# Kernel tuning notes

Measured on AMD Instinct MI355X. Metric: run time of the kernel, lower is better.

Reference implementation:

```python
import jax, jax.numpy as jnp
import numpy as np

B, N, M = 8, 8192, 2048
C1, C2 = 128, 256
MLP = [256, 128]
EPS_W = 1e-8   # inverse-distance epsilon
EPS_BN = 1e-5  # batchnorm epsilon


def setup_inputs() -> dict:
    key = jax.random.key(0)
    ks = jax.random.split(key, 12)
    inp = {
        "xyz1": jax.random.normal(ks[0], (B, N, 3), jnp.float32),
        "xyz2": jax.random.normal(ks[1], (B, M, 3), jnp.float32),
        "points1": jax.random.normal(ks[2], (B, N, C1), jnp.float32),
        "points2": jax.random.normal(ks[3], (B, M, C2), jnp.float32),
    }
    last = C1 + C2
    for i, out_c in enumerate(MLP):
        inp[f"W{i}"] = jax.random.normal(ks[4 + 2 * i], (out_c, last), jnp.float32) * (1.0 / np.sqrt(last))
        inp[f"b{i}"] = jnp.zeros((out_c,), jnp.float32)
        inp[f"gamma{i}"] = jnp.ones((out_c,), jnp.float32)
        inp[f"beta{i}"] = jnp.zeros((out_c,), jnp.float32)
        last = out_c
    return inp


def _square_distance(src, dst):
    # [B,N,M] squared euclidean distances
    d = -2.0 * jnp.einsum("bnc,bmc->bnm", src, dst)
    d = d + jnp.sum(src * src, -1)[:, :, None]
    d = d + jnp.sum(dst * dst, -1)[:, None, :]
    return d


def _fp_forward(xyz1, xyz2, points1, points2, params):
    dists = _square_distance(xyz1, xyz2)              # [B,N,M]
    neg_top, idx = jax.lax.top_k(-dists, 3)            # 3 smallest distances
    d3 = -neg_top                                      # [B,N,3]
    recip = 1.0 / (d3 + EPS_W)
    weight = recip / jnp.sum(recip, axis=2, keepdims=True)  # [B,N,3]
    gathered = jax.vmap(lambda p, i: p[i])(points2, idx)     # [B,N,3,C2]
    interpolated = jnp.sum(gathered * weight[..., None], axis=2)  # [B,N,C2]
    x = jnp.concatenate([points1, interpolated], axis=-1)        # [B,N,C1+C2]
    for (Wi, bi, gi, bti) in params:
        x = jnp.einsum("bnc,oc->bno", x, Wi) + bi
        # BatchNorm1d (training mode): stats over batch and point dims
        mean = jnp.mean(x, axis=(0, 1))
        var = jnp.var(x, axis=(0, 1))
        x = (x - mean) * jax.lax.rsqrt(var + EPS_BN) * gi + bti
        x = jax.nn.relu(x)
    return x  # [B,N,MLP[-1]]


def reference(xyz1, xyz2, points1, points2, W0, b0, gamma0, beta0, W1, b1, gamma1, beta1):
    params = [(W0, b0, gamma0, beta0), (W1, b1, gamma1, beta1)]
    return _fp_forward(xyz1, xyz2, points1, points2, params)
```

## Files before the change

kernel.cpp:

```cpp
#include <hip/hip_runtime.h>
#include <cstdint>
#include <cstddef>

#define BATCH 8
#define NPTS  8192
#define MPTS  2048
#define C1    128
#define C2    256
#define K0    384
#define O0    256
#define O1    128
#define NROWS (BATCH * NPTS)

typedef __attribute__((ext_vector_type(8))) short bf16x8;
typedef __attribute__((ext_vector_type(4))) float f32x4;

__device__ __forceinline__ unsigned short f2b(float f) {
    union { float f; unsigned int u; } v; v.f = f;
    unsigned int u = v.u + 0x7FFFu + ((v.u >> 16) & 1u);
    return (unsigned short)(u >> 16);
}
__device__ __forceinline__ float b2f(unsigned short h) {
    union { unsigned int u; float f; } v; v.u = ((unsigned int)h) << 16; return v.f;
}
__device__ __forceinline__ unsigned int pack2(float a, float b) {
    return (unsigned int)f2b(a) | ((unsigned int)f2b(b) << 16);
}
__device__ __forceinline__ float med3(float a, float b, float c) {
    return __builtin_amdgcn_fmed3f(a, b, c);
}

__device__ __forceinline__ void merge3(float x0, float x1, float x2,
                                       int ix0, int ix1, int ix2,
                                       float y0, float y1, float y2,
                                       int iy0, int iy1, int iy2,
                                       float& z0, float& z1, float& z2,
                                       int& iz0, int& iz1, int& iz2) {
    const bool c0 = y0 < x0;
    const bool c1a = y1 < x0;
    const bool c1b = y0 < x1;
    z0 = c0 ? y0 : x0;  iz0 = c0 ? iy0 : ix0;
    const float z1A = c1a ? y1 : x0; const int iz1A = c1a ? iy1 : ix0;
    const float z1B = c1b ? y0 : x1; const int iz1B = c1b ? iy0 : ix1;
    z1 = c0 ? z1A : z1B; iz1 = c0 ? iz1A : iz1B;
    const bool mA1c = y2 < x0;
    const bool mA2c = y1 < x1;
    const bool mB2c = y0 < x2;
    const float mA1 = mA1c ? y2 : x0; const int imA1 = mA1c ? iy2 : ix0;
    const float mA2 = mA2c ? y1 : x1; const int imA2 = mA2c ? iy1 : ix1;
    const float mB2 = mB2c ? y0 : x2; const int imB2 = mB2c ? iy0 : ix2;
    const float z2A = c1a ? mA1 : mA2; const int iz2A = c1a ? imA1 : imA2;
    const float z2B = c1b ? mA2 : mB2; const int iz2B = c1b ? imA2 : imB2;
    z2 = c0 ? z2A : z2B; iz2 = c0 ? iz2A : iz2B;
}

__global__ __launch_bounds__(512) void k_knn(const float* __restrict__ xyz1,
                                             const float* __restrict__ xyz2,
                                             int* __restrict__ idxo,
                                             float* __restrict__ wo) {
    __shared__ float4 s2p[16][129];

    const int b = blockIdx.x >> 7;
    const int qbase = (blockIdx.x & 127) * 64;

    for (int p = threadIdx.x; p < MPTS; p += 512) {
        const size_t src = ((size_t)b * MPTS + p) * 3;
        float px = xyz2[src + 0], py = xyz2[src + 1], pz = xyz2[src + 2];
        float sy = __fadd_rn(__fadd_rn(__fmul_rn(px, px), __fmul_rn(py, py)),
                             __fmul_rn(pz, pz));
        s2p[p >> 7][p & 127] = make_float4(-2.0f * px, -2.0f * py, -2.0f * pz, sy);
    }
    __syncthreads();

    const int qp  = threadIdx.x >> 4;
    const int seg = threadIdx.x & 15;
    const int nA = qbase + qp * 2;
    const size_t qoffA = ((size_t)b * NPTS + nA) * 3;
    const float ax = xyz1[qoffA + 0], ay = xyz1[qoffA + 1], az = xyz1[qoffA + 2];
    const float bx = xyz1[qoffA + 3], by = xyz1[qoffA + 4], bz = xyz1[qoffA + 5];
    const float sA = __fadd_rn(__fadd_rn(__fmul_rn(ax, ax), __fmul_rn(ay, ay)),
                               __fmul_rn(az, az));
    const float sB = __fadd_rn(__fadd_rn(__fmul_rn(bx, bx), __fmul_rn(by, by)),
                               __fmul_rn(bz, bz));

    float a0 = 3.0e38f, a1 = 3.0e38f, a2 = 3.0e38f;
    float e0 = 3.0e38f, e1 = 3.0e38f, e2 = 3.0e38f;
    int ai0 = 0, ai1 = 0, ai2 = 0;
    int bi0 = 0, bi1 = 0, bi2 = 0;
    const int m0 = seg * 128;
    const float4* segp = &s2p[seg][0];
#pragma unroll 8
    for (int mm = 0; mm < 128; ++mm) {
        const float4 pp = segp[mm];
        float tA = __fadd_rn(__fadd_rn(__fmul_rn(ax, pp.x), __fmul_rn(ay, pp.y)),
                             __fmul_rn(az, pp.z));
        float dA = __fadd_rn(__fadd_rn(tA, sA), pp.w);
        float tB = __fadd_rn(__fadd_rn(__fmul_rn(bx, pp.x), __fmul_rn(by, pp.y)),
                             __fmul_rn(bz, pp.z));
        float dB = __fadd_rn(__fadd_rn(tB, sB), pp.w);
        {
            const bool c0 = dA < a0, c1 = dA < a1, c2 = dA < a2;
            ai2 = c2 ? (c1 ? ai1 : mm) : ai2;
            ai1 = c1 ? (c0 ? ai0 : mm) : ai1;
            ai0 = c0 ? mm : ai0;
            float n2 = med3(dA, a1, a2), n1 = med3(dA, a0, a1), n0 = fminf(dA, a0);
            a2 = n2; a1 = n1; a0 = n0;
        }
        {
            const bool c0 = dB < e0, c1 = dB < e1, c2 = dB < e2;
            bi2 = c2 ? (c1 ? bi1 : mm) : bi2;
            bi1 = c1 ? (c0 ? bi0 : mm) : bi1;
            bi0 = c0 ? mm : bi0;
            float n2 = med3(dB, e1, e2), n1 = med3(dB, e0, e1), n0 = fminf(dB, e0);
            e2 = n2; e1 = n1; e0 = n0;
        }
    }
    ai0 += m0; ai1 += m0; ai2 += m0;
    bi0 += m0; bi1 += m0; bi2 += m0;

#pragma unroll
    for (int k = 1; k <= 8; k <<= 1) {
        const bool up = (threadIdx.x & k) != 0;
        {
            float p0 = __shfl_xor(a0, k), p1 = __shfl_xor(a1, k), p2 = __shfl_xor(a2, k);
            int   q0 = __shfl_xor(ai0, k), q1 = __shfl_xor(ai1, k), q2 = __shfl_xor(ai2, k);
            float x0 = up ? p0 : a0, x1 = up ? p1 : a1, x2 = up ? p2 : a2;
            int  ix0 = up ? q0 : ai0, ix1 = up ? q1 : ai1, ix2 = up ? q2 : ai2;
            float y0 = up ? a0 : p0, y1 = up ? a1 : p1, y2 = up ? a2 : p2;
            int  iy0 = up ? ai0 : q0, iy1 = up ? ai1 : q1, iy2 = up ? ai2 : q2;
            merge3(x0, x1, x2, ix0, ix1, ix2, y0, y1, y2, iy0, iy1, iy2,
                   a0, a1, a2, ai0, ai1, ai2);
        }
        {
            float p0 = __shfl_xor(e0, k), p1 = __shfl_xor(e1, k), p2 = __shfl_xor(e2, k);
            int   q0 = __shfl_xor(bi0, k), q1 = __shfl_xor(bi1, k), q2 = __shfl_xor(bi2, k);
            float x0 = up ? p0 : e0, x1 = up ? p1 : e1, x2 = up ? p2 : e2;
            int  ix0 = up ? q0 : bi0, ix1 = up ? q1 : bi1, ix2 = up ? q2 : bi2;
            float y0 = up ? e0 : p0, y1 = up ? e1 : p1, y2 = up ? e2 : p2;
            int  iy0 = up ? bi0 : q0, iy1 = up ? bi1 : q1, iy2 = up ? bi2 : q2;
            merge3(x0, x1, x2, ix0, ix1, ix2, y0, y1, y2, iy0, iy1, iy2,
                   e0, e1, e2, bi0, bi1, bi2);
        }
    }

    if (seg == 0) {
        {
            const float r0 = 1.0f / __fadd_rn(a0, 1e-8f);
            const float r1 = 1.0f / __fadd_rn(a1, 1e-8f);
            const float r2 = 1.0f / __fadd_rn(a2, 1e-8f);
            const float norm = __fadd_rn(__fadd_rn(r0, r1), r2);
            const size_t row = (size_t)b * NPTS + nA;
            idxo[row * 3 + 0] = ai0; idxo[row * 3 + 1] = ai1; idxo[row * 3 + 2] = ai2;
            wo[row * 3 + 0] = r0 / norm;
            wo[row * 3 + 1] = r1 / norm;
            wo[row * 3 + 2] = r2 / norm;
        }
        {
            const float r0 = 1.0f / __fadd_rn(e0, 1e-8f);
            const float r1 = 1.0f / __fadd_rn(e1, 1e-8f);
            const float r2 = 1.0f / __fadd_rn(e2, 1e-8f);
            const float norm = __fadd_rn(__fadd_rn(r0, r1), r2);
            const size_t row = (size_t)b * NPTS + nA + 1;
            idxo[row * 3 + 0] = bi0; idxo[row * 3 + 1] = bi1; idxo[row * 3 + 2] = bi2;
            wo[row * 3 + 0] = r0 / norm;
            wo[row * 3 + 1] = r1 / norm;
            wo[row * 3 + 2] = r2 / norm;
        }
    }
}

__global__ __launch_bounds__(256) void k_cvt(const float* __restrict__ W0,
                                             const float* __restrict__ W1,
                                             unsigned short* __restrict__ Wb0,
                                             unsigned short* __restrict__ Wb1) {
    const int e = blockIdx.x * 256 + threadIdx.x;
    if (e < O0 * K0) Wb0[e] = f2b(W0[e]);
    const int e2 = e - O0 * K0;
    if (e2 >= 0 && e2 < O1 * O0) Wb1[e2] = f2b(W1[e2]);
}

__global__ __launch_bounds__(512) void k_gemm0(const float* __restrict__ p1,
                                               const float* __restrict__ p2,
                                               const int* __restrict__ idx,
                                               const float* __restrict__ w,
                                               const unsigned short* __restrict__ Wb,
                                               const float* __restrict__ bias,
                                               unsigned short* __restrict__ y,
                                               float* __restrict__ ps,
                                               float* __restrict__ pq) {
    __shared__ __align__(16) unsigned short As[128 * 64];
    __shared__ __align__(16) unsigned short Bs[256 * 64];
    __shared__ float cps[2][256][2];
    const int t = threadIdx.x;
    const int r0 = blockIdx.x * 128;
    const int lane = t & 63;
    const int wid = t >> 6;
    const int wm = wid & 1;
    const int wn = wid >> 1;

    const int row_a = t >> 2;
    const int sa0 = (t & 3) * 2;
    const int row_b = t >> 1;
    const int sb0 = (t & 1) * 4;

    const int grow = r0 + row_a;
    const int bb = grow >> 13;
    const int i0 = idx[grow * 3 + 0];
    const int i1 = idx[grow * 3 + 1];
    const int i2 = idx[grow * 3 + 2];
    const float w0 = w[grow * 3 + 0];
    const float w1 = w[grow * 3 + 1];
    const float w2 = w[grow * 3 + 2];
    const float* pbase = p2 + (size_t)bb * MPTS * C2;
    const float* g0 = pbase + (size_t)i0 * C2;
    const float* g1 = pbase + (size_t)i1 * C2;
    const float* g2 = pbase + (size_t)i2 * C2;
    const float* p1row = p1 + (size_t)grow * C1;

    const unsigned short* bptr = Wb + (size_t)row_b * K0;
    unsigned short* asw = &As[row_a * 64];
    unsigned short* bsw = &Bs[row_b * 64];
    const int swa = row_a & 7;
    const int swb = row_b & 7;

    f32x4 zero = {0.f, 0.f, 0.f, 0.f};
    f32x4 acc[4][4];
#pragma unroll
    for (int i = 0; i < 4; ++i)
#pragma unroll
        for (int j = 0; j < 4; ++j) acc[i][j] = zero;

    for (int kt = 0; kt < K0; kt += 64) {
#pragma unroll
        for (int i = 0; i < 2; ++i) {
            const int slot = sa0 + i;
            const int gc = kt + slot * 8;
            uint4 ov;
            if (kt < C1) {
                const float4 u = *(const float4*)&p1row[gc];
                const float4 v = *(const float4*)&p1row[gc + 4];
                ov.x = pack2(u.x, u.y); ov.y = pack2(u.z, u.w);
                ov.z = pack2(v.x, v.y); ov.w = pack2(v.z, v.w);
            } else {
                const int cc = gc - C1;
                const float4 u0 = *(const float4*)&g0[cc];
                const float4 u1 = *(const float4*)&g0[cc + 4];
                const float4 v0 = *(const float4*)&g1[cc];
                const float4 v1 = *(const float4*)&g1[cc + 4];
                const float4 t0 = *(const float4*)&g2[cc];
                const float4 t1 = *(const float4*)&g2[cc + 4];
                const float f0 = w0 * u0.x + w1 * v0.x + w2 * t0.x;
                const float f1 = w0 * u0.y + w1 * v0.y + w2 * t0.y;
                const float f2 = w0 * u0.z + w1 * v0.z + w2 * t0.z;
                const float f3 = w0 * u0.w + w1 * v0.w + w2 * t0.w;
                const float f4 = w0 * u1.x + w1 * v1.x + w2 * t1.x;
                const float f5 = w0 * u1.y + w1 * v1.y + w2 * t1.y;
                const float f6 = w0 * u1.z + w1 * v1.z + w2 * t1.z;
                const float f7 = w0 * u1.w + w1 * v1.w + w2 * t1.w;
                ov.x = pack2(f0, f1); ov.y = pack2(f2, f3);
                ov.z = pack2(f4, f5); ov.w = pack2(f6, f7);
            }
            *(uint4*)(asw + ((slot ^ swa) * 8)) = ov;
        }
#pragma unroll
        for (int i = 0; i < 4; ++i) {
            const int slot = sb0 + i;
            *(uint4*)(bsw + (slot ^ swb) * 8) = *(const uint4*)(bptr + kt + slot * 8);
        }
        __syncthreads();
#pragma unroll
        for (int ks = 0; ks < 2; ++ks) {
            bf16x8 af[4], bfr[4];
#pragma unroll
            for (int fr = 0; fr < 4; ++fr) {
                const int row = wm * 64 + fr * 16 + (lane & 15);
                const int slot = (ks * 4 + (lane >> 4)) ^ (row & 7);
                af[fr] = *(const bf16x8*)&As[row * 64 + slot * 8];
            }
#pragma unroll
            for (int fc = 0; fc < 4; ++fc) {
                const int row = wn * 64 + fc * 16 + (lane & 15);
                const int slot = (ks * 4 + (lane >> 4)) ^ (row & 7);
                bfr[fc] = *(const bf16x8*)&Bs[row * 64 + slot * 8];
            }
#pragma unroll
            for (int fr = 0; fr < 4; ++fr)
#pragma unroll
                for (int fc = 0; fc < 4; ++fc)
                    acc[fr][fc] = __builtin_amdgcn_mfma_f32_16x16x32_bf16(
                        af[fr], bfr[fc], acc[fr][fc], 0, 0, 0);
        }
        __syncthreads();
    }

    float bv[4];
#pragma unroll
    for (int fc = 0; fc < 4; ++fc) {
        const int n = wn * 64 + fc * 16 + (lane & 15);
        bv[fc] = bias[n];
        float s = 0.0f, q = 0.0f;
#pragma unroll
        for (int fr = 0; fr < 4; ++fr) {
#pragma unroll
            for (int j = 0; j < 4; ++j) {
                const float v = b2f(f2b(acc[fr][fc][j] + bv[fc]));
                s += v;
                q = fmaf(v, v, q);
            }
        }
        s += __shfl_xor(s, 16); s += __shfl_xor(s, 32);
        q += __shfl_xor(q, 16); q += __shfl_xor(q, 32);
        if ((lane >> 4) == 0) { cps[wm][n][0] = s; cps[wm][n][1] = q; }
    }
    __syncthreads();
    if (t < 256) {
        const float s = cps[0][t][0] + cps[1][t][0];
        const float q = cps[0][t][1] + cps[1][t][1];
        const size_t o = (size_t)blockIdx.x * 256 + t;
        ps[o] = s; pq[o] = q;
    }

#pragma unroll
    for (int p = 0; p < 2; ++p) {
        __syncthreads();
        if (wm == p) {
#pragma unroll
            for (int fc = 0; fc < 4; ++fc) {
                const int n = wn * 64 + fc * 16 + (lane & 15);
#pragma unroll
                for (int fr = 0; fr < 4; ++fr) {
#pragma unroll
                    for (int j = 0; j < 4; ++j) {
                        const int lr = fr * 16 + (lane >> 4) * 4 + j;
                        Bs[lr * 256 + n] = f2b(acc[fr][fc][j] + bv[fc]);
                    }
                }
            }
        }
        __syncthreads();
        const int lr2 = t >> 3;
        const int cb = (t & 7);
#pragma unroll
        for (int i = 0; i < 4; ++i) {
            const int col = (cb + i * 8) * 8;
            *(uint4*)&y[(size_t)(r0 + p * 64 + lr2) * O0 + col] =
                *(const uint4*)&Bs[lr2 * 256 + col];
        }
    }
}

__global__ __launch_bounds__(256) void k_fin0(const float* __restrict__ ps,
                                              const float* __restrict__ pq,
                                              const float* __restrict__ gamma,
                                              const float* __restrict__ beta,
                                              float* __restrict__ sc,
                                              float* __restrict__ sh) {
    __shared__ float red[8][32][2];
    const int tid = threadIdx.x;
    const int cl = tid & 31, qr = tid >> 5;
    const int c = blockIdx.x * 32 + cl;
    float s = 0.0f, q = 0.0f;
    for (int bx = qr * 64; bx < qr * 64 + 64; ++bx) {
        s += ps[(size_t)bx * 256 + c];
        q += pq[(size_t)bx * 256 + c];
    }
    red[qr][cl][0] = s; red[qr][cl][1] = q;
    __syncthreads();
    if (tid < 32) {
        float ss = 0.0f, qq = 0.0f;
#pragma unroll
        for (int k = 0; k < 8; ++k) { ss += red[k][tid][0]; qq += red[k][tid][1]; }
        const int ch = blockIdx.x * 32 + tid;
        const float mean = ss * (1.0f / NROWS);
        const float var = qq * (1.0f / NROWS) - mean * mean;
        const float rs = rsqrtf(var + 1e-5f);
        const float scale = gamma[ch] * rs;
        sc[ch] = scale;
        sh[ch] = beta[ch] - mean * scale;
    }
}

__global__ __launch_bounds__(256) void k_gemm1(const unsigned short* __restrict__ y0,
                                               const unsigned short* __restrict__ Wb,
                                               const float* __restrict__ bias,
                                               const float* __restrict__ sc,
                                               const float* __restrict__ sh,
                                               unsigned short* __restrict__ y1,
                                               float* __restrict__ ps,
                                               float* __restrict__ pq) {
    __shared__ __align__(16) unsigned short As[128 * 64];
    __shared__ __align__(16) unsigned short Bs[128 * 64];
    __shared__ float cps[2][128][2];
    const int t = threadIdx.x;
    const int r0 = blockIdx.x * 128;
    const int lane = t & 63;
    const int wm = (t >> 6) & 1;
    const int wn = (t >> 6) >> 1;
    const int row_s = t >> 1;
    const int slot4 = (t & 1) * 4;
    const int sw = row_s & 7;

    const unsigned short* aptr = y0 + (size_t)(r0 + row_s) * O0;
    const unsigned short* bptr = Wb + (size_t)row_s * O0;
    unsigned short* asw = &As[row_s * 64];
    unsigned short* bsw = &Bs[row_s * 64];

    f32x4 zero = {0.f, 0.f, 0.f, 0.f};
    f32x4 acc[4][4];
#pragma unroll
    for (int i = 0; i < 4; ++i)
#pragma unroll
        for (int j = 0; j < 4; ++j) acc[i][j] = zero;

    for (int kt = 0; kt < O0; kt += 64) {
#pragma unroll
        for (int i = 0; i < 4; ++i) {
            const int slot = slot4 + i;
            const int ssw = slot ^ sw;
            const int c0 = kt + slot * 8;
            uint4 av = *(const uint4*)(aptr + c0);
            const float4 s0 = *(const float4*)&sc[c0];
            const float4 s1 = *(const float4*)&sc[c0 + 4];
            const float4 h0 = *(const float4*)&sh[c0];
            const float4 h1 = *(const float4*)&sh[c0 + 4];
            uint4 ov;
            {
                float v0 = b2f(av.x & 0xffff), v1 = b2f(av.x >> 16);
                ov.x = pack2(fmaxf(fmaf(v0, s0.x, h0.x), 0.f),
                             fmaxf(fmaf(v1, s0.y, h0.y), 0.f));
                float v2 = b2f(av.y & 0xffff), v3 = b2f(av.y >> 16);
                ov.y = pack2(fmaxf(fmaf(v2, s0.z, h0.z), 0.f),
                             fmaxf(fmaf(v3, s0.w, h0.w), 0.f));
                float v4 = b2f(av.z & 0xffff), v5 = b2f(av.z >> 16);
                ov.z = pack2(fmaxf(fmaf(v4, s1.x, h1.x), 0.f),
                             fmaxf(fmaf(v5, s1.y, h1.y), 0.f));
                float v6 = b2f(av.w & 0xffff), v7 = b2f(av.w >> 16);
                ov.w = pack2(fmaxf(fmaf(v6, s1.z, h1.z), 0.f),
                             fmaxf(fmaf(v7, s1.w, h1.w), 0.f));
            }
            *(uint4*)(asw + ssw * 8) = ov;
            uint4 bv = *(const uint4*)(bptr + c0);
            *(uint4*)(bsw + ssw * 8) = bv;
        }
        __syncthreads();
#pragma unroll
        for (int ks = 0; ks < 2; ++ks) {
            bf16x8 af[4], bfr[4];
#pragma unroll
            for (int fr = 0; fr < 4; ++fr) {
                const int row = wm * 64 + fr * 16 + (lane & 15);
                const int slot = (ks * 4 + (lane >> 4)) ^ (row & 7);
                af[fr] = *(const bf16x8*)&As[row * 64 + slot * 8];
            }
#pragma unroll
            for (int fc = 0; fc < 4; ++fc) {
                const int row = wn * 64 + fc * 16 + (lane & 15);
                const int slot = (ks * 4 + (lane >> 4)) ^ (row & 7);
                bfr[fc] = *(const bf16x8*)&Bs[row * 64 + slot * 8];
            }
#pragma unroll
            for (int fr = 0; fr < 4; ++fr)
#pragma unroll
                for (int fc = 0; fc < 4; ++fc)
                    acc[fr][fc] = __builtin_amdgcn_mfma_f32_16x16x32_bf16(
                        af[fr], bfr[fc], acc[fr][fc], 0, 0, 0);
        }
        __syncthreads();
    }

    float bvr[4];
#pragma unroll
    for (int fc = 0; fc < 4; ++fc) {
        const int cl = wn * 64 + fc * 16 + (lane & 15);
        bvr[fc] = bias[cl];
        float s = 0.0f, q = 0.0f;
#pragma unroll
        for (int fr = 0; fr < 4; ++fr) {
#pragma unroll
            for (int j = 0; j < 4; ++j) {
                const float v = b2f(f2b(acc[fr][fc][j] + bvr[fc]));
                s += v;
                q = fmaf(v, v, q);
            }
        }
        s += __shfl_xor(s, 16); s += __shfl_xor(s, 32);
        q += __shfl_xor(q, 16); q += __shfl_xor(q, 32);
        if ((lane >> 4) == 0) { cps[wm][cl][0] = s; cps[wm][cl][1] = q; }
    }
    __syncthreads();
    if (t < 128) {
        ps[(size_t)blockIdx.x * 128 + t] = cps[0][t][0] + cps[1][t][0];
        pq[(size_t)blockIdx.x * 128 + t] = cps[0][t][1] + cps[1][t][1];
    }

#pragma unroll
    for (int p = 0; p < 2; ++p) {
        __syncthreads();
        if (wm == p) {
#pragma unroll
            for (int fc = 0; fc < 4; ++fc) {
                const int cl = wn * 64 + fc * 16 + (lane & 15);
#pragma unroll
                for (int fr = 0; fr < 4; ++fr) {
#pragma unroll
                    for (int j = 0; j < 4; ++j) {
                        const int lr = fr * 16 + (lane >> 4) * 4 + j;
                        Bs[lr * 128 + cl] = f2b(acc[fr][fc][j] + bvr[fc]);
                    }
                }
            }
        }
        __syncthreads();
        const int lr2 = t >> 2;
        const int cb = (t & 3);
#pragma unroll
        for (int i = 0; i < 4; ++i) {
            const int col = (cb + i * 4) * 8;
            *(uint4*)&y1[(size_t)(r0 + p * 64 + lr2) * O1 + col] =
                *(const uint4*)&Bs[lr2 * 128 + col];
        }
    }
}

__global__ __launch_bounds__(128) void k_fin1(const float* __restrict__ ps,
                                              const float* __restrict__ pq,
                                              const float* __restrict__ gamma,
                                              const float* __restrict__ beta,
                                              float* __restrict__ sc,
                                              float* __restrict__ sh) {
    __shared__ float red[8][16][2];
    const int tid = threadIdx.x;
    const int cl = tid & 15, qr = tid >> 4;
    const int c = blockIdx.x * 16 + cl;
    float s = 0.0f, q = 0.0f;
    for (int bx = qr * 64; bx < qr * 64 + 64; ++bx) {
        s += ps[(size_t)bx * 128 + c];
        q += pq[(size_t)bx * 128 + c];
    }
    red[qr][cl][0] = s; red[qr][cl][1] = q;
    __syncthreads();
    if (tid < 16) {
        float ss = 0.0f, qq = 0.0f;
#pragma unroll
        for (int k = 0; k < 8; ++k) { ss += red[k][tid][0]; qq += red[k][tid][1]; }
        const int ch = blockIdx.x * 16 + tid;
        const float mean = ss * (1.0f / NROWS);
        const float var = qq * (1.0f / NROWS) - mean * mean;
        const float rs = rsqrtf(var + 1e-5f);
        const float scale = gamma[ch] * rs;
        sc[ch] = scale;
        sh[ch] = beta[ch] - mean * scale;
    }
}

__global__ __launch_bounds__(256) void k_bnrelu(const unsigned short* __restrict__ y1,
                                                const float* __restrict__ sc,
                                                const float* __restrict__ sh,
                                                float* __restrict__ out) {
    const int e8 = blockIdx.x * 256 + threadIdx.x;
    const int c = (e8 & 15) << 3;
    const uint4 v = ((const uint4*)y1)[e8];
    float4 lo, hi;
    const float4 s0 = *(const float4*)&sc[c];
    const float4 s1 = *(const float4*)&sc[c + 4];
    const float4 h0 = *(const float4*)&sh[c];
    const float4 h1 = *(const float4*)&sh[c + 4];
    lo.x = fmaxf(fmaf(b2f(v.x & 0xffff), s0.x, h0.x), 0.0f);
    lo.y = fmaxf(fmaf(b2f(v.x >> 16),    s0.y, h0.y), 0.0f);
    lo.z = fmaxf(fmaf(b2f(v.y & 0xffff), s0.z, h0.z), 0.0f);
    lo.w = fmaxf(fmaf(b2f(v.y >> 16),    s0.w, h0.w), 0.0f);
    hi.x = fmaxf(fmaf(b2f(v.z & 0xffff), s1.x, h1.x), 0.0f);
    hi.y = fmaxf(fmaf(b2f(v.z >> 16),    s1.y, h1.y), 0.0f);
    hi.z = fmaxf(fmaf(b2f(v.w & 0xffff), s1.z, h1.z), 0.0f);
    hi.w = fmaxf(fmaf(b2f(v.w >> 16),    s1.w, h1.w), 0.0f);
    ((float4*)out)[(size_t)e8 * 2 + 0] = lo;
    ((float4*)out)[(size_t)e8 * 2 + 1] = hi;
}

extern "C" void kernel_launch(void* const* d_in, const int* in_sizes, int n_in,
                              void* d_out, int out_size, void* d_ws, size_t ws_size,
                              hipStream_t stream) {
    const float* xyz1    = (const float*)d_in[0];
    const float* xyz2    = (const float*)d_in[1];
    const float* points1 = (const float*)d_in[2];
    const float* points2 = (const float*)d_in[3];
    const float* W0      = (const float*)d_in[4];
    const float* b0      = (const float*)d_in[5];
    const float* gamma0  = (const float*)d_in[6];
    const float* beta0   = (const float*)d_in[7];
    const float* W1      = (const float*)d_in[8];
    const float* b1      = (const float*)d_in[9];
    const float* gamma1  = (const float*)d_in[10];
    const float* beta1   = (const float*)d_in[11];
    float* out = (float*)d_out;

    char* ws = (char*)d_ws;
    unsigned short* y0  = (unsigned short*)(ws + 0);
    unsigned short* y1b = (unsigned short*)(ws + 33554432ull);
    int*            idxb= (int*)           (ws + 50331648ull);
    float*          wb  = (float*)         (ws + 51118080ull);
    unsigned short* Wb0 = (unsigned short*)(ws + 51904512ull);
    unsigned short* Wb1 = (unsigned short*)(ws + 52101120ull);
    float*          ps0 = (float*)         (ws + 52166656ull);
    float*          pq0 = (float*)         (ws + 52690944ull);
    float*          ps1 = (float*)         (ws + 53215232ull);
    float*          pq1 = (float*)         (ws + 53477376ull);
    float*          sc0 = (float*)         (ws + 53739520ull);
    float*          sh0 = (float*)         (ws + 53740544ull);
    float*          sc1 = (float*)         (ws + 53741568ull);
    float*          sh1 = (float*)         (ws + 53742080ull);

    hipLaunchKernelGGL(k_cvt, dim3(512), dim3(256), 0, stream, W0, W1, Wb0, Wb1);
    hipLaunchKernelGGL(k_knn, dim3(1024), dim3(512), 0, stream, xyz1, xyz2,
                       idxb, wb);
    hipLaunchKernelGGL(k_gemm0, dim3(NROWS / 128), dim3(512), 0, stream,
                       points1, points2, idxb, wb, Wb0, b0, y0, ps0, pq0);
    hipLaunchKernelGGL(k_fin0, dim3(8), dim3(256), 0, stream,
                       ps0, pq0, gamma0, beta0, sc0, sh0);
    hipLaunchKernelGGL(k_gemm1, dim3(NROWS / 128), dim3(256), 0, stream,
                       y0, Wb1, b1, sc0, sh0, y1b, ps1, pq1);
    hipLaunchKernelGGL(k_fin1, dim3(8), dim3(128), 0, stream,
                       ps1, pq1, gamma1, beta1, sc1, sh1);
    hipLaunchKernelGGL(k_bnrelu, dim3(NROWS * O1 / 8 / 256), dim3(256), 0, stream,
                       y1b, sc1, sh1, out);
}
```

Baseline: 161.7 us.

## Fuse KNN search into first GEMM and convert weights to bf16 on the fly

The separate KNN kernel is folded into the prologue of k_gemm0: each 128-row block loads all xyz2 points of its batch into shared memory, computes the 3 nearest neighbours and weights for its rows, and keeps idx/weights in shared memory instead of going through global memory. The k_cvt weight-conversion kernel is removed, and both GEMMs read fp32 weights and pack them to bf16 while staging tiles. This saves two launches and the idx/weight round trip. In exchange, each block now does more KNN work per thread (8 segments of 256 instead of 16 of 128), the GEMM grid of 512 blocks runs the KNN with less parallelism, and weight conversion is repeated in every block.

```diff
diff --git a/kernel.cpp b/kernel.cpp
--- a/kernel.cpp
+++ b/kernel.cpp
@@ -54,145 +54,135 @@
     z2 = c0 ? z2A : z2B; iz2 = c0 ? iz2A : iz2B;
 }
 
-__global__ __launch_bounds__(512) void k_knn(const float* __restrict__ xyz1,
-                                             const float* __restrict__ xyz2,
-                                             int* __restrict__ idxo,
-                                             float* __restrict__ wo) {
-    __shared__ float4 s2p[16][129];
-
-    const int b = blockIdx.x >> 7;
-    const int qbase = (blockIdx.x & 127) * 64;
-
-    for (int p = threadIdx.x; p < MPTS; p += 512) {
-        const size_t src = ((size_t)b * MPTS + p) * 3;
-        float px = xyz2[src + 0], py = xyz2[src + 1], pz = xyz2[src + 2];
-        float sy = __fadd_rn(__fadd_rn(__fmul_rn(px, px), __fmul_rn(py, py)),
-                             __fmul_rn(pz, pz));
-        s2p[p >> 7][p & 127] = make_float4(-2.0f * px, -2.0f * py, -2.0f * pz, sy);
-    }
-    __syncthreads();
-
-    const int qp  = threadIdx.x >> 4;
-    const int seg = threadIdx.x & 15;
-    const int nA = qbase + qp * 2;
-    const size_t qoffA = ((size_t)b * NPTS + nA) * 3;
-    const float ax = xyz1[qoffA + 0], ay = xyz1[qoffA + 1], az = xyz1[qoffA + 2];
-    const float bx = xyz1[qoffA + 3], by = xyz1[qoffA + 4], bz = xyz1[qoffA + 5];
-    const float sA = __fadd_rn(__fadd_rn(__fmul_rn(ax, ax), __fmul_rn(ay, ay)),
-                               __fmul_rn(az, az));
-    const float sB = __fadd_rn(__fadd_rn(__fmul_rn(bx, bx), __fmul_rn(by, by)),
-                               __fmul_rn(bz, bz));
-
-    float a0 = 3.0e38f, a1 = 3.0e38f, a2 = 3.0e38f;
-    float e0 = 3.0e38f, e1 = 3.0e38f, e2 = 3.0e38f;
-    int ai0 = 0, ai1 = 0, ai2 = 0;
-    int bi0 = 0, bi1 = 0, bi2 = 0;
-    const int m0 = seg * 128;
-    const float4* segp = &s2p[seg][0];
-#pragma unroll 8
-    for (int mm = 0; mm < 128; ++mm) {
-        const float4 pp = segp[mm];
-        float tA = __fadd_rn(__fadd_rn(__fmul_rn(ax, pp.x), __fmul_rn(ay, pp.y)),
-                             __fmul_rn(az, pp.z));
-        float dA = __fadd_rn(__fadd_rn(tA, sA), pp.w);
-        float tB = __fadd_rn(__fadd_rn(__fmul_rn(bx, pp.x), __fmul_rn(by, pp.y)),
-                             __fmul_rn(bz, pp.z));
-        float dB = __fadd_rn(__fadd_rn(tB, sB), pp.w);
-        {
-            const bool c0 = dA < a0, c1 = dA < a1, c2 = dA < a2;
-            ai2 = c2 ? (c1 ? ai1 : mm) : ai2;
-            ai1 = c1 ? (c0 ? ai0 : mm) : ai1;
-            ai0 = c0 ? mm : ai0;
-            float n2 = med3(dA, a1, a2), n1 = med3(dA, a0, a1), n0 = fminf(dA, a0);
-            a2 = n2; a1 = n1; a0 = n0;
-        }
-        {
-            const bool c0 = dB < e0, c1 = dB < e1, c2 = dB < e2;
-            bi2 = c2 ? (c1 ? bi1 : mm) : bi2;
-            bi1 = c1 ? (c0 ? bi0 : mm) : bi1;
-            bi0 = c0 ? mm : bi0;
-            float n2 = med3(dB, e1, e2), n1 = med3(dB, e0, e1), n0 = fminf(dB, e0);
-            e2 = n2; e1 = n1; e0 = n0;
-        }
-    }
-    ai0 += m0; ai1 += m0; ai2 += m0;
-    bi0 += m0; bi1 += m0; bi2 += m0;
-
-#pragma unroll
-    for (int k = 1; k <= 8; k <<= 1) {
-        const bool up = (threadIdx.x & k) != 0;
-        {
-            float p0 = __shfl_xor(a0, k), p1 = __shfl_xor(a1, k), p2 = __shfl_xor(a2, k);
-            int   q0 = __shfl_xor(ai0, k), q1 = __shfl_xor(ai1, k), q2 = __shfl_xor(ai2, k);
-            float x0 = up ? p0 : a0, x1 = up ? p1 : a1, x2 = up ? p2 : a2;
-            int  ix0 = up ? q0 : ai0, ix1 = up ? q1 : ai1, ix2 = up ? q2 : ai2;
-            float y0 = up ? a0 : p0, y1 = up ? a1 : p1, y2 = up ? a2 : p2;
-            int  iy0 = up ? ai0 : q0, iy1 = up ? ai1 : q1, iy2 = up ? ai2 : q2;
-            merge3(x0, x1, x2, ix0, ix1, ix2, y0, y1, y2, iy0, iy1, iy2,
-                   a0, a1, a2, ai0, ai1, ai2);
-        }
-        {
-            float p0 = __shfl_xor(e0, k), p1 = __shfl_xor(e1, k), p2 = __shfl_xor(e2, k);
-            int   q0 = __shfl_xor(bi0, k), q1 = __shfl_xor(bi1, k), q2 = __shfl_xor(bi2, k);
-            float x0 = up ? p0 : e0, x1 = up ? p1 : e1, x2 = up ? p2 : e2;
-            int  ix0 = up ? q0 : bi0, ix1 = up ? q1 : bi1, ix2 = up ? q2 : bi2;
-            float y0 = up ? e0 : p0, y1 = up ? e1 : p1, y2 = up ? e2 : p2;
-            int  iy0 = up ? bi0 : q0, iy1 = up ? bi1 : q1, iy2 = up ? bi2 : q2;
-            merge3(x0, x1, x2, ix0, ix1, ix2, y0, y1, y2, iy0, iy1, iy2,
-                   e0, e1, e2, bi0, bi1, bi2);
-        }
-    }
-
-    if (seg == 0) {
-        {
-            const float r0 = 1.0f / __fadd_rn(a0, 1e-8f);
-            const float r1 = 1.0f / __fadd_rn(a1, 1e-8f);
-            const float r2 = 1.0f / __fadd_rn(a2, 1e-8f);
-            const float norm = __fadd_rn(__fadd_rn(r0, r1), r2);
-            const size_t row = (size_t)b * NPTS + nA;
-            idxo[row * 3 + 0] = ai0; idxo[row * 3 + 1] = ai1; idxo[row * 3 + 2] = ai2;
-            wo[row * 3 + 0] = r0 / norm;
-            wo[row * 3 + 1] = r1 / norm;
-            wo[row * 3 + 2] = r2 / norm;
-        }
-        {
-            const float r0 = 1.0f / __fadd_rn(e0, 1e-8f);
-            const float r1 = 1.0f / __fadd_rn(e1, 1e-8f);
-            const float r2 = 1.0f / __fadd_rn(e2, 1e-8f);
-            const float norm = __fadd_rn(__fadd_rn(r0, r1), r2);
-            const size_t row = (size_t)b * NPTS + nA + 1;
-            idxo[row * 3 + 0] = bi0; idxo[row * 3 + 1] = bi1; idxo[row * 3 + 2] = bi2;
-            wo[row * 3 + 0] = r0 / norm;
-            wo[row * 3 + 1] = r1 / norm;
-            wo[row * 3 + 2] = r2 / norm;
-        }
-    }
-}
-
-__global__ __launch_bounds__(256) void k_cvt(const float* __restrict__ W0,
-                                             const float* __restrict__ W1,
-                                             unsigned short* __restrict__ Wb0,
-                                             unsigned short* __restrict__ Wb1) {
-    const int e = blockIdx.x * 256 + threadIdx.x;
-    if (e < O0 * K0) Wb0[e] = f2b(W0[e]);
-    const int e2 = e - O0 * K0;
-    if (e2 >= 0 && e2 < O1 * O0) Wb1[e2] = f2b(W1[e2]);
-}
-
-__global__ __launch_bounds__(512) void k_gemm0(const float* __restrict__ p1,
+__global__ __launch_bounds__(512) void k_gemm0(const float* __restrict__ xyz1,
+                                               const float* __restrict__ xyz2,
+                                               const float* __restrict__ p1,
                                                const float* __restrict__ p2,
-                                               const int* __restrict__ idx,
-                                               const float* __restrict__ w,
-                                               const unsigned short* __restrict__ Wb,
+                                               const float* __restrict__ W0f,
                                                const float* __restrict__ bias,
                                                unsigned short* __restrict__ y,
                                                float* __restrict__ ps,
                                                float* __restrict__ pq) {
-    __shared__ __align__(16) unsigned short As[128 * 64];
-    __shared__ __align__(16) unsigned short Bs[256 * 64];
-    __shared__ float cps[2][256][2];
+    __shared__ __align__(16) char smem[49152 + 3072];
+    float4*         s2p = (float4*)smem;
+    unsigned short* As  = (unsigned short*)smem;
+    unsigned short* Bs  = (unsigned short*)(smem + 16384);
+    float*          cps = (float*)smem;
+    int*            lidx = (int*)(smem + 49152);
+    float*          lw   = (float*)(smem + 49152 + 1536);
+
     const int t = threadIdx.x;
     const int r0 = blockIdx.x * 128;
+    const int bb = r0 >> 13;
+
+    for (int p = t; p < MPTS; p += 512) {
+        const size_t src = ((size_t)bb * MPTS + p) * 3;
+        float px = xyz2[src + 0], py = xyz2[src + 1], pz = xyz2[src + 2];
+        float sy = __fadd_rn(__fadd_rn(__fmul_rn(px, px), __fmul_rn(py, py)),
+                             __fmul_rn(pz, pz));
+        s2p[(p >> 8) * 257 + (p & 255)] =
+            make_float4(-2.0f * px, -2.0f * py, -2.0f * pz, sy);
+    }
+    __syncthreads();
+
+    {
+        const int qp  = t >> 3;
+        const int seg = t & 7;
+        const size_t qoffA = ((size_t)r0 + qp * 2) * 3;
+        const float ax = xyz1[qoffA + 0], ay = xyz1[qoffA + 1], az = xyz1[qoffA + 2];
+        const float bx = xyz1[qoffA + 3], by = xyz1[qoffA + 4], bz = xyz1[qoffA + 5];
+        const float sA = __fadd_rn(__fadd_rn(__fmul_rn(ax, ax), __fmul_rn(ay, ay)),
+                                   __fmul_rn(az, az));
+        const float sB = __fadd_rn(__fadd_rn(__fmul_rn(bx, bx), __fmul_rn(by, by)),
+                                   __fmul_rn(bz, bz));
+
+        float a0 = 3.0e38f, a1 = 3.0e38f, a2 = 3.0e38f;
+        float e0 = 3.0e38f, e1 = 3.0e38f, e2 = 3.0e38f;
+        int ai0 = 0, ai1 = 0, ai2 = 0;
+        int bi0 = 0, bi1 = 0, bi2 = 0;
+        const float4* segp = &s2p[seg * 257];
+#pragma unroll 8
+        for (int mm = 0; mm < 256; ++mm) {
+            const float4 pp = segp[mm];
+            float tA = __fadd_rn(__fadd_rn(__fmul_rn(ax, pp.x), __fmul_rn(ay, pp.y)),
+                                 __fmul_rn(az, pp.z));
+            float dA = __fadd_rn(__fadd_rn(tA, sA), pp.w);
+            float tB = __fadd_rn(__fadd_rn(__fmul_rn(bx, pp.x), __fmul_rn(by, pp.y)),
+                                 __fmul_rn(bz, pp.z));
+            float dB = __fadd_rn(__fadd_rn(tB, sB), pp.w);
+            {
+                const bool c0 = dA < a0, c1 = dA < a1, c2 = dA < a2;
+                ai2 = c2 ? (c1 ? ai1 : mm) : ai2;
+                ai1 = c1 ? (c0 ? ai0 : mm) : ai1;
+                ai0 = c0 ? mm : ai0;
+                float n2 = med3(dA, a1, a2), n1 = med3(dA, a0, a1), n0 = fminf(dA, a0);
+                a2 = n2; a1 = n1; a0 = n0;
+            }
+            {
+                const bool c0 = dB < e0, c1 = dB < e1, c2 = dB < e2;
+                bi2 = c2 ? (c1 ? bi1 : mm) : bi2;
+                bi1 = c1 ? (c0 ? bi0 : mm) : bi1;
+                bi0 = c0 ? mm : bi0;
+                float n2 = med3(dB, e1, e2), n1 = med3(dB, e0, e1), n0 = fminf(dB, e0);
+                e2 = n2; e1 = n1; e0 = n0;
+            }
+        }
+        const int m0 = seg * 256;
+        ai0 += m0; ai1 += m0; ai2 += m0;
+        bi0 += m0; bi1 += m0; bi2 += m0;
+
+#pragma unroll
+        for (int k = 1; k <= 4; k <<= 1) {
+            const bool up = (t & k) != 0;
+            {
+                float p0 = __shfl_xor(a0, k), p1v = __shfl_xor(a1, k), p2v = __shfl_xor(a2, k);
+                int   q0 = __shfl_xor(ai0, k), q1 = __shfl_xor(ai1, k), q2 = __shfl_xor(ai2, k);
+                float x0 = up ? p0 : a0, x1 = up ? p1v : a1, x2 = up ? p2v : a2;
+                int  ix0 = up ? q0 : ai0, ix1 = up ? q1 : ai1, ix2 = up ? q2 : ai2;
+                float y0 = up ? a0 : p0, y1 = up ? a1 : p1v, y2 = up ? a2 : p2v;
+                int  iy0 = up ? ai0 : q0, iy1 = up ? ai1 : q1, iy2 = up ? ai2 : q2;
+                merge3(x0, x1, x2, ix0, ix1, ix2, y0, y1, y2, iy0, iy1, iy2,
+                       a0, a1, a2, ai0, ai1, ai2);
+            }
+            {
+                float p0 = __shfl_xor(e0, k), p1v = __shfl_xor(e1, k), p2v = __shfl_xor(e2, k);
+                int   q0 = __shfl_xor(bi0, k), q1 = __shfl_xor(bi1, k), q2 = __shfl_xor(bi2, k);
+                float x0 = up ? p0 : e0, x1 = up ? p1v : e1, x2 = up ? p2v : e2;
+                int  ix0 = up ? q0 : bi0, ix1 = up ? q1 : bi1, ix2 = up ? q2 : bi2;
+                float y0 = up ? e0 : p0, y1 = up ? e1 : p1v, y2 = up ? e2 : p2v;
+                int  iy0 = up ? bi0 : q0, iy1 = up ? bi1 : q1, iy2 = up ? bi2 : q2;
+                merge3(x0, x1, x2, ix0, ix1, ix2, y0, y1, y2, iy0, iy1, iy2,
+                       e0, e1, e2, bi0, bi1, bi2);
+            }
+        }
+
+        if (seg == 0) {
+            {
+                const float rr0 = 1.0f / __fadd_rn(a0, 1e-8f);
+                const float rr1 = 1.0f / __fadd_rn(a1, 1e-8f);
+                const float rr2 = 1.0f / __fadd_rn(a2, 1e-8f);
+                const float norm = __fadd_rn(__fadd_rn(rr0, rr1), rr2);
+                const int lr = qp * 2;
+                lidx[lr * 3 + 0] = ai0; lidx[lr * 3 + 1] = ai1; lidx[lr * 3 + 2] = ai2;
+                lw[lr * 3 + 0] = rr0 / norm;
+                lw[lr * 3 + 1] = rr1 / norm;
+                lw[lr * 3 + 2] = rr2 / norm;
+            }
+            {
+                const float rr0 = 1.0f / __fadd_rn(e0, 1e-8f);
+                const float rr1 = 1.0f / __fadd_rn(e1, 1e-8f);
+                const float rr2 = 1.0f / __fadd_rn(e2, 1e-8f);
+                const float norm = __fadd_rn(__fadd_rn(rr0, rr1), rr2);
+                const int lr = qp * 2 + 1;
+                lidx[lr * 3 + 0] = bi0; lidx[lr * 3 + 1] = bi1; lidx[lr * 3 + 2] = bi2;
+                lw[lr * 3 + 0] = rr0 / norm;
+                lw[lr * 3 + 1] = rr1 / norm;
+                lw[lr * 3 + 2] = rr2 / norm;
+            }
+        }
+    }
+    __syncthreads();
+
     const int lane = t & 63;
     const int wid = t >> 6;
     const int wm = wid & 1;
@@ -204,20 +194,19 @@
     const int sb0 = (t & 1) * 4;
 
     const int grow = r0 + row_a;
-    const int bb = grow >> 13;
-    const int i0 = idx[grow * 3 + 0];
-    const int i1 = idx[grow * 3 + 1];
-    const int i2 = idx[grow * 3 + 2];
-    const float w0 = w[grow * 3 + 0];
-    const float w1 = w[grow * 3 + 1];
-    const float w2 = w[grow * 3 + 2];
+    const int i0 = lidx[row_a * 3 + 0];
+    const int i1 = lidx[row_a * 3 + 1];
+    const int i2 = lidx[row_a * 3 + 2];
+    const float w0 = lw[row_a * 3 + 0];
+    const float w1 = lw[row_a * 3 + 1];
+    const float w2 = lw[row_a * 3 + 2];
     const float* pbase = p2 + (size_t)bb * MPTS * C2;
     const float* g0 = pbase + (size_t)i0 * C2;
     const float* g1 = pbase + (size_t)i1 * C2;
     const float* g2 = pbase + (size_t)i2 * C2;
     const float* p1row = p1 + (size_t)grow * C1;
 
-    const unsigned short* bptr = Wb + (size_t)row_b * K0;
+    const float* bwp = W0f + (size_t)row_b * K0;
     unsigned short* asw = &As[row_a * 64];
     unsigned short* bsw = &Bs[row_b * 64];
     const int swa = row_a & 7;
@@ -265,7 +254,13 @@
 #pragma unroll
         for (int i = 0; i < 4; ++i) {
             const int slot = sb0 + i;
-            *(uint4*)(bsw + (slot ^ swb) * 8) = *(const uint4*)(bptr + kt + slot * 8);
+            const int gc = kt + slot * 8;
+            const float4 u = *(const float4*)&bwp[gc];
+            const float4 v = *(const float4*)&bwp[gc + 4];
+            uint4 ov;
+            ov.x = pack2(u.x, u.y); ov.y = pack2(u.z, u.w);
+            ov.z = pack2(v.x, v.y); ov.w = pack2(v.z, v.w);
+            *(uint4*)(bsw + (slot ^ swb) * 8) = ov;
         }
         __syncthreads();
 #pragma unroll
@@ -310,12 +305,15 @@
         }
         s += __shfl_xor(s, 16); s += __shfl_xor(s, 32);
         q += __shfl_xor(q, 16); q += __shfl_xor(q, 32);
-        if ((lane >> 4) == 0) { cps[wm][n][0] = s; cps[wm][n][1] = q; }
+        if ((lane >> 4) == 0) {
+            cps[((wm * 256 + n) << 1) + 0] = s;
+            cps[((wm * 256 + n) << 1) + 1] = q;
+        }
     }
     __syncthreads();
     if (t < 256) {
-        const float s = cps[0][t][0] + cps[1][t][0];
-        const float q = cps[0][t][1] + cps[1][t][1];
+        const float s = cps[((0 * 256 + t) << 1) + 0] + cps[((1 * 256 + t) << 1) + 0];
+        const float q = cps[((0 * 256 + t) << 1) + 1] + cps[((1 * 256 + t) << 1) + 1];
         const size_t o = (size_t)blockIdx.x * 256 + t;
         ps[o] = s; pq[o] = q;
     }
@@ -381,7 +379,7 @@
 }
 
 __global__ __launch_bounds__(256) void k_gemm1(const unsigned short* __restrict__ y0,
-                                               const unsigned short* __restrict__ Wb,
+                                               const float* __restrict__ W1f,
                                                const float* __restrict__ bias,
                                                const float* __restrict__ sc,
                                                const float* __restrict__ sh,
@@ -401,7 +399,7 @@
     const int sw = row_s & 7;
 
     const unsigned short* aptr = y0 + (size_t)(r0 + row_s) * O0;
-    const unsigned short* bptr = Wb + (size_t)row_s * O0;
+    const float* bptr = W1f + (size_t)row_s * O0;
     unsigned short* asw = &As[row_s * 64];
     unsigned short* bsw = &Bs[row_s * 64];
 
@@ -439,8 +437,12 @@
                              fmaxf(fmaf(v7, s1.w, h1.w), 0.f));
             }
             *(uint4*)(asw + ssw * 8) = ov;
-            uint4 bv = *(const uint4*)(bptr + c0);
-            *(uint4*)(bsw + ssw * 8) = bv;
+            const float4 u = *(const float4*)&bptr[c0];
+            const float4 v = *(const float4*)&bptr[c0 + 4];
+            uint4 bvv;
+            bvv.x = pack2(u.x, u.y); bvv.y = pack2(u.z, u.w);
+            bvv.z = pack2(v.x, v.y); bvv.w = pack2(v.z, v.w);
+            *(uint4*)(bsw + ssw * 8) = bvv;
         }
         __syncthreads();
 #pragma unroll
@@ -597,28 +599,21 @@
     char* ws = (char*)d_ws;
     unsigned short* y0  = (unsigned short*)(ws + 0);
     unsigned short* y1b = (unsigned short*)(ws + 33554432ull);
-    int*            idxb= (int*)           (ws + 50331648ull);
-    float*          wb  = (float*)         (ws + 51118080ull);
-    unsigned short* Wb0 = (unsigned short*)(ws + 51904512ull);
-    unsigned short* Wb1 = (unsigned short*)(ws + 52101120ull);
-    float*          ps0 = (float*)         (ws + 52166656ull);
-    float*          pq0 = (float*)         (ws + 52690944ull);
-    float*          ps1 = (float*)         (ws + 53215232ull);
-    float*          pq1 = (float*)         (ws + 53477376ull);
-    float*          sc0 = (float*)         (ws + 53739520ull);
-    float*          sh0 = (float*)         (ws + 53740544ull);
-    float*          sc1 = (float*)         (ws + 53741568ull);
-    float*          sh1 = (float*)         (ws + 53742080ull);
-
-    hipLaunchKernelGGL(k_cvt, dim3(512), dim3(256), 0, stream, W0, W1, Wb0, Wb1);
-    hipLaunchKernelGGL(k_knn, dim3(1024), dim3(512), 0, stream, xyz1, xyz2,
-                       idxb, wb);
+    float*          ps0 = (float*)         (ws + 50331648ull);
+    float*          pq0 = (float*)         (ws + 50855936ull);
+    float*          ps1 = (float*)         (ws + 51380224ull);
+    float*          pq1 = (float*)         (ws + 51642368ull);
+    float*          sc0 = (float*)         (ws + 51904512ull);
+    float*          sh0 = (float*)         (ws + 51905536ull);
+    float*          sc1 = (float*)         (ws + 51906560ull);
+    float*          sh1 = (float*)         (ws + 51907072ull);
+
     hipLaunchKernelGGL(k_gemm0, dim3(NROWS / 128), dim3(512), 0, stream,
-                       points1, points2, idxb, wb, Wb0, b0, y0, ps0, pq0);
+                       xyz1, xyz2, points1, points2, W0, b0, y0, ps0, pq0);
     hipLaunchKernelGGL(k_fin0, dim3(8), dim3(256), 0, stream,
                        ps0, pq0, gamma0, beta0, sc0, sh0);
     hipLaunchKernelGGL(k_gemm1, dim3(NROWS / 128), dim3(256), 0, stream,
-                       y0, Wb1, b1, sc0, sh0, y1b, ps1, pq1);
+                       y0, W1, b1, sc0, sh0, y1b, ps1, pq1);
     hipLaunchKernelGGL(k_fin1, dim3(8), dim3(128), 0, stream,
                        ps1, pq1, gamma1, beta1, sc1, sh1);
     hipLaunchKernelGGL(k_bnrelu, dim3(NROWS * O1 / 8 / 256), dim3(256), 0, stream,
```

After: 178.4 us. 1.1x slower.
